# Kernel tuning notes

Hardware: AMD Instinct MI355X
Metric: run time of the kernel (lower is better)

Reference implementation:

```python
import jax, jax.numpy as jnp
import numpy as np
import math

N_CELLS = 8192
IN_DIM = 64
HID = 128
OUT_DIM = 64
MAX_AGE = 50.0
TOP_K = 8


def faction_sync_debate(h, step, n_factions=8, sync_strength=0.15, debate_strength=0.15):
    n, d = h.shape
    n_f = min(n_factions, n // 2)
    if n_f < 2:
        return h
    fs = n // n_f
    used = n_f * fs
    body = h[:used].reshape(n_f, fs, d)
    fmean = body.mean(axis=1, keepdims=True)                 # per-faction mean
    body = (1.0 - sync_strength) * body + sync_strength * fmean
    if step > 5:
        global_op = body.mean(axis=1).mean(axis=0)           # [d]
        dc = max(1, fs // 4)
        body = body.at[:, :dc].set((1.0 - debate_strength) * body[:, :dc] + debate_strength * global_op)
    out = body.reshape(used, d)
    if used < n:
        out = jnp.concatenate([out, h[used:]], axis=0)
    return out


def setup_inputs() -> dict:
    key = jax.random.key(0)
    ks = jax.random.split(key, 10)

    def lin(k, fin, fout):
        kw, kb = jax.random.split(k)
        s = 1.0 / math.sqrt(fin)
        w = jax.random.uniform(kw, (fout, fin), minval=-s, maxval=s, dtype=jnp.float32)
        b = jax.random.uniform(kb, (fout,), minval=-s, maxval=s, dtype=jnp.float32)
        return w, b

    in_w, in_b = lin(ks[0], IN_DIM, HID)
    out_w, out_b = lin(ks[1], HID, IN_DIM)
    ea_w1, ea_b1 = lin(ks[2], HID, 128)
    ea_w2, ea_b2 = lin(ks[3], 128, OUT_DIM)
    eg_w1, eg_b1 = lin(ks[4], HID, 128)
    eg_w2, eg_b2 = lin(ks[5], 128, OUT_DIM)
    prototypes = jax.random.normal(ks[6], (N_CELLS, HID), dtype=jnp.float32) * 0.3
    # sparse random topology state (evolved-state stand-in for the zero-init buffers)
    edges = (jax.random.uniform(ks[7], (N_CELLS, N_CELLS)) < 0.001).astype(jnp.float32)
    edges = jnp.maximum(edges, edges.T)
    edge_ages = jax.random.randint(ks[8], (N_CELLS, N_CELLS), 0, 60).astype(jnp.float32) * edges
    x = jax.random.normal(ks[9], (1, IN_DIM), dtype=jnp.float32)
    return dict(x=x, step=10, prototypes=prototypes, edges=edges, edge_ages=edge_ages,
                in_w=in_w, in_b=in_b, out_w=out_w, out_b=out_b,
                ea_w1=ea_w1, ea_b1=ea_b1, ea_w2=ea_w2, ea_b2=ea_b2,
                eg_w1=eg_w1, eg_b1=eg_b1, eg_w2=eg_w2, eg_b2=eg_b2)


def reference(x, step, prototypes, edges, edge_ages, in_w, in_b, out_w, out_b,
              ea_w1, ea_b1, ea_w2, ea_b2, eg_w1, eg_b1, eg_w2, eg_b2):
    signal = (x @ in_w.T + in_b)[0]                          # [HID]
    # ---- torch.no_grad() region: GNG competitive update ----
    sgp = jax.lax.stop_gradient(prototypes)
    sgs = jax.lax.stop_gradient(signal)
    dists = jnp.sum((sgp - sgs[None, :]) ** 2, axis=-1)      # [N]
    sorted_idx = jnp.argsort(dists)
    bmu1, bmu2 = sorted_idx[0], sorted_idx[1]
    eps_w = max(0.05, 0.3 * math.exp(-step / 200.0))
    eps_n = eps_w * 0.01
    proto = sgp.at[bmu1].add(eps_w * (sgs - sgp[bmu1]))
    proto = proto.at[bmu2].add(eps_n * (sgs - proto[bmu2]))
    e = edges.at[bmu1, bmu2].set(1.0).at[bmu2, bmu1].set(1.0)
    ages = edge_ages.at[bmu1, bmu2].set(0.0).at[bmu2, bmu1].set(0.0)
    ages = ages.at[bmu1, :].add(1.0).at[:, bmu1].add(1.0)
    old = ages > MAX_AGE
    e = jnp.where(old, 0.0, e)
    ages = jnp.where(old, 0.0, ages)
    # vectorized neighbor EMA (replaces per-neighbor python loop; rows independent)
    nmask = (e[bmu1] > 0).astype(proto.dtype)                # [N]
    proto = proto + eps_n * nmask[:, None] * (sgs[None, :] - proto)
    proto = faction_sync_debate(proto, step)
    # value = updated prototypes, grad = identity to the prototypes parameter
    # (torch mutates .data in-place, then reads the Parameter directly)
    proto_used = prototypes + jax.lax.stop_gradient(proto - prototypes)
    # ---- differentiable head ----
    winner_h = proto_used[bmu1][None, :]                     # [1, HID]
    a_out = jax.nn.relu(winner_h @ ea_w1.T + ea_b1) @ ea_w2.T + ea_b2
    g_out = jax.nn.relu(winner_h @ eg_w1.T + eg_b1) @ eg_w2.T + eg_b2
    tension = jnp.mean((a_out - g_out) ** 2)
    top_idx = sorted_idx[:TOP_K]
    weights = jax.nn.softmax(-dists[top_idx])                # [K]
    combined = jnp.sum(weights[:, None] * proto_used[top_idx], axis=0, keepdims=True)
    output = combined @ out_w.T + out_b                      # [1, IN_DIM]
    return output, tension
```

## Files before the change

### kernel.cpp

```cpp
#include <hip/hip_runtime.h>
#include <math.h>

#define N_CELLS 8192
#define HIDDIM 128
#define IN_DIM 64
#define TOPK 8


__global__ void k_init(float* __restrict__ z) {
    int t = blockIdx.x * blockDim.x + threadIdx.x;
    if (t < 2056) z[t] = 0.0f;
}

__global__ __launch_bounds__(128) void k_signal(const float* __restrict__ x,
                                                const float* __restrict__ in_w,
                                                const float* __restrict__ in_b,
                                                float* __restrict__ signal) {
    int j = threadIdx.x;
    float acc = in_b[j];
    const float* w = in_w + j * IN_DIM;
    #pragma unroll
    for (int k = 0; k < IN_DIM; ++k) acc += x[k] * w[k];
    signal[j] = acc;
}

__global__ __launch_bounds__(256) void k_dist(const float* __restrict__ proto,
                                              const float* __restrict__ signal,
                                              float* __restrict__ dists,
                                              float* __restrict__ fsum0) {
    __shared__ float sm[4 * 128];
    int tid = threadIdx.x;
    int wave = tid >> 6, lane = tid & 63;
    float2 s2 = ((const float2*)signal)[lane];
    float fx = 0.0f, fy = 0.0f;
    int base = blockIdx.x * 64;
    for (int c = wave; c < 64; c += 4) {
        int cell = base + c;
        float2 p = ((const float2*)(proto + (size_t)cell * HIDDIM))[lane];
        float dx = p.x - s2.x, dy = p.y - s2.y;
        float d = dx * dx + dy * dy;
        #pragma unroll
        for (int off = 32; off > 0; off >>= 1) d += __shfl_down(d, off, 64);
        if (lane == 0) dists[cell] = d;
        fx += p.x; fy += p.y;
    }
    sm[wave * 128 + 2 * lane]     = fx;
    sm[wave * 128 + 2 * lane + 1] = fy;
    __syncthreads();
    if (tid < 128) {
        float s = sm[tid] + sm[128 + tid] + sm[256 + tid] + sm[384 + tid];
        int f = blockIdx.x >> 4;
        atomicAdd(&fsum0[f * HIDDIM + tid], s);
    }
}

__global__ __launch_bounds__(256) void k_top8(const float* __restrict__ dists,
                                              float* __restrict__ topdist,
                                              int* __restrict__ topidx) {
    __shared__ float sd[N_CELLS];
    __shared__ float sv[256];
    __shared__ int   si[256];
    int tid = threadIdx.x;
    for (int j = 0; j < 32; ++j) sd[j * 256 + tid] = dists[j * 256 + tid];
    __syncthreads();
    for (int k = 0; k < TOPK; ++k) {
        float lv = INFINITY; int li = N_CELLS;
        #pragma unroll
        for (int j = 0; j < 32; ++j) {
            int   ii = j * 256 + tid;
            float vv = sd[ii];
            if (vv < lv || (vv == lv && ii < li)) { lv = vv; li = ii; }
        }
        sv[tid] = lv; si[tid] = li;
        __syncthreads();
        for (int s = 128; s > 0; s >>= 1) {
            if (tid < s) {
                float ov = sv[tid + s]; int oi = si[tid + s];
                if (ov < sv[tid] || (ov == sv[tid] && oi < si[tid])) { sv[tid] = ov; si[tid] = oi; }
            }
            __syncthreads();
        }
        if (tid == 0) {
            topdist[k] = sv[0];
            topidx[k]  = si[0];
            sd[si[0]]  = INFINITY;
        }
        __syncthreads();
    }
}

__global__ __launch_bounds__(256) void k_coef(const float* __restrict__ proto,
                                              const float* __restrict__ edges,
                                              const float* __restrict__ ages,
                                              const int* __restrict__ step_p,
                                              const int* __restrict__ topidx,
                                              float* __restrict__ acoef,
                                              float* __restrict__ csum,
                                              float* __restrict__ Bf) {
    int i = blockIdx.x * blockDim.x + threadIdx.x;
    if (i >= N_CELLS) return;
    int bmu1 = topidx[0], bmu2 = topidx[1];
    float step = (float)step_p[0];
    float eps_w = fmaxf(0.05f, 0.3f * expf(-step / 200.0f));
    float eps_n = eps_w * 0.01f;

    size_t ro = (size_t)bmu1 * N_CELLS + (size_t)i;
    float age, ec;
    if (i == bmu2)      { age = 1.0f;             ec = 1.0f; }
    else if (i == bmu1) { age = ages[ro] + 2.0f;  ec = edges[ro]; }
    else                { age = ages[ro] + 1.0f;  ec = edges[ro]; }
    bool nb = ((age > 50.0f) ? 0.0f : ec) > 0.0f;

    float a = 1.0f;
    if (i == bmu1) a *= (1.0f - eps_w);
    if (i == bmu2) a *= (1.0f - eps_n);
    if (nb)        a *= (1.0f - eps_n);
    acoef[i] = a;

    if (a != 1.0f) {
        int f = i >> 10;
        const float* p = proto + (size_t)i * HIDDIM;
        for (int d = 0; d < HIDDIM; ++d)
            atomicAdd(&csum[f * HIDDIM + d], (a - 1.0f) * p[d]);
        atomicAdd(&Bf[f], 1.0f - a);
    }
}

__global__ __launch_bounds__(128) void k_final(const float* __restrict__ proto,
                                               const float* __restrict__ signal,
                                               const float* __restrict__ acoef,
                                               const float* __restrict__ fsum0,
                                               const float* __restrict__ csum,
                                               const float* __restrict__ Bf,
                                               const float* __restrict__ topdist,
                                               const int* __restrict__ topidx,
                                               const int* __restrict__ step_p,
                                               const float* __restrict__ ea_w1,
                                               const float* __restrict__ ea_b1,
                                               const float* __restrict__ ea_w2,
                                               const float* __restrict__ ea_b2,
                                               const float* __restrict__ eg_w1,
                                               const float* __restrict__ eg_b1,
                                               const float* __restrict__ eg_w2,
                                               const float* __restrict__ eg_b2,
                                               const float* __restrict__ out_w,
                                               const float* __restrict__ out_b,
                                               float* __restrict__ d_out) {
    __shared__ float wh[128], cmb[128], hA[128], hG[128];
    int d = threadIdx.x;
    int step = step_p[0];
    float s = signal[d];

    float fm[8]; float g = 0.0f;
    #pragma unroll
    for (int f = 0; f < 8; ++f) {
        float v = (fsum0[f * 128 + d] + csum[f * 128 + d] + Bf[f] * s) * (1.0f / 1024.0f);
        fm[f] = v; g += v;
    }
    g *= (1.0f / 8.0f);

    float w[TOPK]; float tot = 0.0f; float m = topdist[0];
    #pragma unroll
    for (int k = 0; k < TOPK; ++k) { w[k] = expf(-(topdist[k] - m)); tot += w[k]; }
    float inv = 1.0f / tot;

    float comb = 0.0f, win = 0.0f;
    #pragma unroll
    for (int k = 0; k < TOPK; ++k) {
        int idx = topidx[k];
        float a  = acoef[idx];
        float p1 = a * proto[(size_t)idx * 128 + d] + (1.0f - a) * s;
        float pf = 0.85f * p1 + 0.15f * fm[idx >> 10];
        if (step > 5 && (idx & 1023) < 256) pf = 0.85f * pf + 0.15f * g;
        comb += (w[k] * inv) * pf;
        if (k == 0) win = pf;
    }
    wh[d] = win; cmb[d] = comb;
    __syncthreads();

    float ha = ea_b1[d], hg = eg_b1[d];
    for (int j = 0; j < 128; ++j) {
        ha += wh[j] * ea_w1[d * 128 + j];
        hg += wh[j] * eg_w1[d * 128 + j];
    }
    hA[d] = fmaxf(ha, 0.0f);
    hG[d] = fmaxf(hg, 0.0f);
    __syncthreads();

    if (d < 64) {
        float ao = ea_b2[d], go = eg_b2[d], ov = out_b[d];
        for (int j = 0; j < 128; ++j) {
            ao += hA[j] * ea_w2[d * 128 + j];
            go += hG[j] * eg_w2[d * 128 + j];
            ov += cmb[j] * out_w[d * 128 + j];
        }
        d_out[d] = ov;
        float diff = ao - go;
        float sq = diff * diff;
        #pragma unroll
        for (int off = 32; off > 0; off >>= 1) sq += __shfl_down(sq, off, 64);
        if (d == 0) d_out[64] = sq * (1.0f / 64.0f);
    }
}

extern "C" void kernel_launch(void* const* d_in, const int* in_sizes, int n_in,
                              void* d_out, int out_size, void* d_ws, size_t ws_size,
                              hipStream_t stream) {
    (void)in_sizes; (void)n_in; (void)out_size; (void)ws_size;
    const float* x      = (const float*)d_in[0];
    const int*   step_p = (const int*)  d_in[1];
    const float* proto  = (const float*)d_in[2];
    const float* edges  = (const float*)d_in[3];
    const float* ages   = (const float*)d_in[4];
    const float* in_w   = (const float*)d_in[5];
    const float* in_b   = (const float*)d_in[6];
    const float* out_w  = (const float*)d_in[7];
    const float* out_b  = (const float*)d_in[8];
    const float* ea_w1  = (const float*)d_in[9];
    const float* ea_b1  = (const float*)d_in[10];
    const float* ea_w2  = (const float*)d_in[11];
    const float* ea_b2  = (const float*)d_in[12];
    const float* eg_w1  = (const float*)d_in[13];
    const float* eg_b1  = (const float*)d_in[14];
    const float* eg_w2  = (const float*)d_in[15];
    const float* eg_b2  = (const float*)d_in[16];

    float* ws     = (float*)d_ws;
    float* signal = ws;
    float* dists  = ws + 128;
    float* acoef  = ws + 8320;
    float* fsum0  = ws + 16512;
    float* csum   = ws + 17536;
    float* Bf     = ws + 18560;
    float* topd   = ws + 18568;
    int*   topi   = (int*)(ws + 18576);
    float* out    = (float*)d_out;

    k_init  <<<dim3(9),   dim3(256), 0, stream>>>(fsum0);
    k_signal<<<dim3(1),   dim3(128), 0, stream>>>(x, in_w, in_b, signal);
    k_dist  <<<dim3(128), dim3(256), 0, stream>>>(proto, signal, dists, fsum0);
    k_top8  <<<dim3(1),   dim3(256), 0, stream>>>(dists, topd, topi);
    k_coef  <<<dim3(32),  dim3(256), 0, stream>>>(proto, edges, ages, step_p, topi, acoef, csum, Bf);
    k_final <<<dim3(1),   dim3(128), 0, stream>>>(proto, signal, acoef, fsum0, csum, Bf, topd, topi, step_p,
                                                  ea_w1, ea_b1, ea_w2, ea_b2,
                                                  eg_w1, eg_b1, eg_w2, eg_b2,
                                                  out_w, out_b, out);
}
```

Measured before the change: 488.9 us.

## Fuse top-k with coefficient pass, replace atomics with compacted neighbor list

Drops the zero-init kernel and the global float atomics. k_dist now writes per-block faction partial sums, and k_final reduces them. Top-8 selection and the neighbor-coefficient scan run in one 512-thread block, which compacts the affected cells into a list with a shared-memory counter. The final kernel rebuilds the faction correction from that list and recomputes the top-k coefficients. It also computes the MLP layers with wave-wide coalesced dot products, trading fewer launches and atomics for more serial work in single-block kernels.

```diff
diff --git a/kernel.cpp b/kernel.cpp
--- a/kernel.cpp
+++ b/kernel.cpp
@@ -2,15 +2,8 @@
 #include <math.h>
 
 #define N_CELLS 8192
-#define HIDDIM 128
-#define IN_DIM 64
 #define TOPK 8
 
-
-__global__ void k_init(float* __restrict__ z) {
-    int t = blockIdx.x * blockDim.x + threadIdx.x;
-    if (t < 2056) z[t] = 0.0f;
-}
 
 __global__ __launch_bounds__(128) void k_signal(const float* __restrict__ x,
                                                 const float* __restrict__ in_w,
@@ -18,25 +11,25 @@
                                                 float* __restrict__ signal) {
     int j = threadIdx.x;
     float acc = in_b[j];
-    const float* w = in_w + j * IN_DIM;
+    const float* w = in_w + j * 64;
     #pragma unroll
-    for (int k = 0; k < IN_DIM; ++k) acc += x[k] * w[k];
+    for (int k = 0; k < 64; ++k) acc += x[k] * w[k];
     signal[j] = acc;
 }
 
 __global__ __launch_bounds__(256) void k_dist(const float* __restrict__ proto,
                                               const float* __restrict__ signal,
                                               float* __restrict__ dists,
-                                              float* __restrict__ fsum0) {
-    __shared__ float sm[4 * 128];
+                                              float* __restrict__ partial) {
+    __shared__ float sm[512];
     int tid = threadIdx.x;
     int wave = tid >> 6, lane = tid & 63;
     float2 s2 = ((const float2*)signal)[lane];
     float fx = 0.0f, fy = 0.0f;
-    int base = blockIdx.x * 64;
-    for (int c = wave; c < 64; c += 4) {
+    int base = blockIdx.x * 32;
+    for (int c = wave; c < 32; c += 4) {
         int cell = base + c;
-        float2 p = ((const float2*)(proto + (size_t)cell * HIDDIM))[lane];
+        float2 p = ((const float2*)(proto + (size_t)cell * 128))[lane];
         float dx = p.x - s2.x, dy = p.y - s2.y;
         float d = dx * dx + dy * dy;
         #pragma unroll
@@ -47,93 +40,87 @@
     sm[wave * 128 + 2 * lane]     = fx;
     sm[wave * 128 + 2 * lane + 1] = fy;
     __syncthreads();
-    if (tid < 128) {
-        float s = sm[tid] + sm[128 + tid] + sm[256 + tid] + sm[384 + tid];
-        int f = blockIdx.x >> 4;
-        atomicAdd(&fsum0[f * HIDDIM + tid], s);
-    }
-}
-
-__global__ __launch_bounds__(256) void k_top8(const float* __restrict__ dists,
-                                              float* __restrict__ topdist,
-                                              int* __restrict__ topidx) {
+    if (tid < 128)
+        partial[blockIdx.x * 128 + tid] = sm[tid] + sm[128 + tid] + sm[256 + tid] + sm[384 + tid];
+}
+
+__global__ __launch_bounds__(512) void k_topcoef(const float* __restrict__ dists_g,
+                                                 const float* __restrict__ edges,
+                                                 const float* __restrict__ ages,
+                                                 const int* __restrict__ step_p,
+                                                 float* __restrict__ topd,
+                                                 int* __restrict__ topi,
+                                                 int* __restrict__ nlist,
+                                                 int* __restrict__ listIdx,
+                                                 float* __restrict__ listA) {
     __shared__ float sd[N_CELLS];
-    __shared__ float sv[256];
-    __shared__ int   si[256];
-    int tid = threadIdx.x;
-    for (int j = 0; j < 32; ++j) sd[j * 256 + tid] = dists[j * 256 + tid];
+    __shared__ float sv[512];
+    __shared__ int   si[512];
+    __shared__ int   sbmu[8];
+    __shared__ int   lcnt;
+    int t = threadIdx.x;
+    if (t == 0) lcnt = 0;
+    for (int j = 0; j < 16; ++j) sd[j * 512 + t] = dists_g[j * 512 + t];
     __syncthreads();
     for (int k = 0; k < TOPK; ++k) {
         float lv = INFINITY; int li = N_CELLS;
         #pragma unroll
-        for (int j = 0; j < 32; ++j) {
-            int   ii = j * 256 + tid;
+        for (int j = 0; j < 16; ++j) {
+            int   ii = j * 512 + t;
             float vv = sd[ii];
             if (vv < lv || (vv == lv && ii < li)) { lv = vv; li = ii; }
         }
-        sv[tid] = lv; si[tid] = li;
+        sv[t] = lv; si[t] = li;
         __syncthreads();
-        for (int s = 128; s > 0; s >>= 1) {
-            if (tid < s) {
-                float ov = sv[tid + s]; int oi = si[tid + s];
-                if (ov < sv[tid] || (ov == sv[tid] && oi < si[tid])) { sv[tid] = ov; si[tid] = oi; }
+        for (int s = 256; s > 0; s >>= 1) {
+            if (t < s) {
+                float ov = sv[t + s]; int oi = si[t + s];
+                if (ov < sv[t] || (ov == sv[t] && oi < si[t])) { sv[t] = ov; si[t] = oi; }
             }
             __syncthreads();
         }
-        if (tid == 0) {
-            topdist[k] = sv[0];
-            topidx[k]  = si[0];
-            sd[si[0]]  = INFINITY;
+        if (t == 0) {
+            topd[k] = sv[0]; topi[k] = si[0]; sbmu[k] = si[0];
+            sd[si[0]] = INFINITY;
         }
         __syncthreads();
     }
-}
-
-__global__ __launch_bounds__(256) void k_coef(const float* __restrict__ proto,
-                                              const float* __restrict__ edges,
-                                              const float* __restrict__ ages,
-                                              const int* __restrict__ step_p,
-                                              const int* __restrict__ topidx,
-                                              float* __restrict__ acoef,
-                                              float* __restrict__ csum,
-                                              float* __restrict__ Bf) {
-    int i = blockIdx.x * blockDim.x + threadIdx.x;
-    if (i >= N_CELLS) return;
-    int bmu1 = topidx[0], bmu2 = topidx[1];
+    int bmu1 = sbmu[0], bmu2 = sbmu[1];
     float step = (float)step_p[0];
     float eps_w = fmaxf(0.05f, 0.3f * expf(-step / 200.0f));
     float eps_n = eps_w * 0.01f;
-
-    size_t ro = (size_t)bmu1 * N_CELLS + (size_t)i;
-    float age, ec;
-    if (i == bmu2)      { age = 1.0f;             ec = 1.0f; }
-    else if (i == bmu1) { age = ages[ro] + 2.0f;  ec = edges[ro]; }
-    else                { age = ages[ro] + 1.0f;  ec = edges[ro]; }
-    bool nb = ((age > 50.0f) ? 0.0f : ec) > 0.0f;
-
-    float a = 1.0f;
-    if (i == bmu1) a *= (1.0f - eps_w);
-    if (i == bmu2) a *= (1.0f - eps_n);
-    if (nb)        a *= (1.0f - eps_n);
-    acoef[i] = a;
-
-    if (a != 1.0f) {
-        int f = i >> 10;
-        const float* p = proto + (size_t)i * HIDDIM;
-        for (int d = 0; d < HIDDIM; ++d)
-            atomicAdd(&csum[f * HIDDIM + d], (a - 1.0f) * p[d]);
-        atomicAdd(&Bf[f], 1.0f - a);
-    }
-}
-
-__global__ __launch_bounds__(128) void k_final(const float* __restrict__ proto,
+    const float* erow = edges + (size_t)bmu1 * N_CELLS;
+    const float* arow = ages  + (size_t)bmu1 * N_CELLS;
+    for (int i = t; i < N_CELLS; i += 512) {
+        float age, ec;
+        if (i == bmu2)      { age = 1.0f;          ec = 1.0f; }
+        else if (i == bmu1) { age = arow[i] + 2.0f; ec = erow[i]; }
+        else                { age = arow[i] + 1.0f; ec = erow[i]; }
+        bool nb = ((age > 50.0f) ? 0.0f : ec) > 0.0f;
+        float a = 1.0f;
+        if (i == bmu1) a *= (1.0f - eps_w);
+        if (i == bmu2) a *= (1.0f - eps_n);
+        if (nb)        a *= (1.0f - eps_n);
+        if (a != 1.0f) {
+            int pos = atomicAdd(&lcnt, 1);
+            listIdx[pos] = i;
+            listA[pos]   = a;
+        }
+    }
+    __syncthreads();
+    if (t == 0) *nlist = lcnt;
+}
+
+__global__ __launch_bounds__(256) void k_final(const float* __restrict__ proto,
                                                const float* __restrict__ signal,
-                                               const float* __restrict__ acoef,
-                                               const float* __restrict__ fsum0,
-                                               const float* __restrict__ csum,
-                                               const float* __restrict__ Bf,
-                                               const float* __restrict__ topdist,
-                                               const int* __restrict__ topidx,
+                                               const float* __restrict__ partial,
+                                               const float* __restrict__ topd_g,
+                                               const int* __restrict__ topi_g,
+                                               const int* __restrict__ nlist,
+                                               const int* __restrict__ listIdx,
+                                               const float* __restrict__ listA,
+                                               const float* __restrict__ edges,
+                                               const float* __restrict__ ages,
                                                const int* __restrict__ step_p,
                                                const float* __restrict__ ea_w1,
                                                const float* __restrict__ ea_b1,
@@ -146,60 +133,122 @@
                                                const float* __restrict__ out_w,
                                                const float* __restrict__ out_b,
                                                float* __restrict__ d_out) {
-    __shared__ float wh[128], cmb[128], hA[128], hG[128];
-    int d = threadIdx.x;
+    __shared__ __align__(16) float csumS[1024];
+    __shared__ __align__(16) float fmS[1024];
+    __shared__ float BfS[8];
+    __shared__ __align__(16) float wh[128];
+    __shared__ __align__(16) float cmb[128];
+    __shared__ __align__(16) float hA[128];
+    __shared__ __align__(16) float hG[128];
+    __shared__ float aout[64], gout[64];
+    __shared__ float tda[8];
+    __shared__ int   tia[8];
+    int t = threadIdx.x;
+    int n = *nlist;
     int step = step_p[0];
-    float s = signal[d];
-
-    float fm[8]; float g = 0.0f;
-    #pragma unroll
-    for (int f = 0; f < 8; ++f) {
-        float v = (fsum0[f * 128 + d] + csum[f * 128 + d] + Bf[f] * s) * (1.0f / 1024.0f);
-        fm[f] = v; g += v;
-    }
-    g *= (1.0f / 8.0f);
-
-    float w[TOPK]; float tot = 0.0f; float m = topdist[0];
-    #pragma unroll
-    for (int k = 0; k < TOPK; ++k) { w[k] = expf(-(topdist[k] - m)); tot += w[k]; }
-    float inv = 1.0f / tot;
-
-    float comb = 0.0f, win = 0.0f;
-    #pragma unroll
-    for (int k = 0; k < TOPK; ++k) {
-        int idx = topidx[k];
-        float a  = acoef[idx];
-        float p1 = a * proto[(size_t)idx * 128 + d] + (1.0f - a) * s;
-        float pf = 0.85f * p1 + 0.15f * fm[idx >> 10];
-        if (step > 5 && (idx & 1023) < 256) pf = 0.85f * pf + 0.15f * g;
-        comb += (w[k] * inv) * pf;
-        if (k == 0) win = pf;
-    }
-    wh[d] = win; cmb[d] = comb;
-    __syncthreads();
-
-    float ha = ea_b1[d], hg = eg_b1[d];
-    for (int j = 0; j < 128; ++j) {
-        ha += wh[j] * ea_w1[d * 128 + j];
-        hg += wh[j] * eg_w1[d * 128 + j];
-    }
-    hA[d] = fmaxf(ha, 0.0f);
-    hG[d] = fmaxf(hg, 0.0f);
-    __syncthreads();
-
-    if (d < 64) {
-        float ao = ea_b2[d], go = eg_b2[d], ov = out_b[d];
-        for (int j = 0; j < 128; ++j) {
-            ao += hA[j] * ea_w2[d * 128 + j];
-            go += hG[j] * eg_w2[d * 128 + j];
-            ov += cmb[j] * out_w[d * 128 + j];
-        }
-        d_out[d] = ov;
-        float diff = ao - go;
+    if (t < 8) { tda[t] = topd_g[t]; tia[t] = topi_g[t]; }
+    if (t < 128) {
+        #pragma unroll
+        for (int f = 0; f < 8; ++f) csumS[f * 128 + t] = 0.0f;
+    }
+    __syncthreads();
+    if (t < 128) {
+        int d = t;
+        for (int e = 0; e < n; ++e) {
+            int idx = listIdx[e]; float a = listA[e];
+            csumS[(idx >> 10) * 128 + d] += (a - 1.0f) * proto[(size_t)idx * 128 + d];
+        }
+    } else if (t < 136) {
+        int f = t - 128; float acc = 0.0f;
+        for (int e = 0; e < n; ++e)
+            if ((listIdx[e] >> 10) == f) acc += 1.0f - listA[e];
+        BfS[f] = acc;
+    }
+    __syncthreads();
+    if (t < 128) {
+        int d = t;
+        float s = signal[d];
+        float g = 0.0f;
+        #pragma unroll
+        for (int f = 0; f < 8; ++f) {
+            float acc = 0.0f;
+            for (int b = 0; b < 32; ++b) acc += partial[(f * 32 + b) * 128 + d];
+            float v = (acc + csumS[f * 128 + d] + BfS[f] * s) * (1.0f / 1024.0f);
+            fmS[f * 128 + d] = v; g += v;
+        }
+        g *= 0.125f;
+        float wk[TOPK]; float tot = 0.0f; float m = tda[0];
+        #pragma unroll
+        for (int k = 0; k < TOPK; ++k) { wk[k] = expf(-(tda[k] - m)); tot += wk[k]; }
+        float inv = 1.0f / tot;
+        int bmu1 = tia[0], bmu2 = tia[1];
+        float stf = (float)step;
+        float eps_w = fmaxf(0.05f, 0.3f * expf(-stf / 200.0f));
+        float eps_n = eps_w * 0.01f;
+        float comb = 0.0f, win = 0.0f;
+        #pragma unroll
+        for (int k = 0; k < TOPK; ++k) {
+            int idx = tia[k];
+            size_t ro = (size_t)bmu1 * N_CELLS + (size_t)idx;
+            float age, ec;
+            if (idx == bmu2)      { age = 1.0f;            ec = 1.0f; }
+            else if (idx == bmu1) { age = ages[ro] + 2.0f;  ec = edges[ro]; }
+            else                  { age = ages[ro] + 1.0f;  ec = edges[ro]; }
+            bool nb = ((age > 50.0f) ? 0.0f : ec) > 0.0f;
+            float a = 1.0f;
+            if (idx == bmu1) a *= (1.0f - eps_w);
+            if (idx == bmu2) a *= (1.0f - eps_n);
+            if (nb)          a *= (1.0f - eps_n);
+            float p1 = a * proto[(size_t)idx * 128 + d] + (1.0f - a) * s;
+            float pf = 0.85f * p1 + 0.15f * fmS[(idx >> 10) * 128 + d];
+            if (step > 5 && (idx & 1023) < 256) pf = 0.85f * pf + 0.15f * g;
+            comb += wk[k] * inv * pf;
+            if (k == 0) win = pf;
+        }
+        wh[d] = win; cmb[d] = comb;
+    }
+    __syncthreads();
+    int wave = t >> 6, lane = t & 63;
+    for (int q = 0; q < 64; ++q) {
+        int task = wave * 64 + q;
+        int row = task & 127;
+        const float* W = (task < 128) ? ea_w1 : eg_w1;
+        float2 wv = ((const float2*)(W + row * 128))[lane];
+        float2 hv = ((const float2*)wh)[lane];
+        float acc = wv.x * hv.x + wv.y * hv.y;
+        #pragma unroll
+        for (int off = 32; off > 0; off >>= 1) acc += __shfl_down(acc, off, 64);
+        if (lane == 0) {
+            float b = (task < 128) ? ea_b1[row] : eg_b1[row];
+            float h = fmaxf(acc + b, 0.0f);
+            if (task < 128) hA[row] = h; else hG[row] = h;
+        }
+    }
+    __syncthreads();
+    for (int q = 0; q < 48; ++q) {
+        int task = wave + 4 * q;
+        int row; const float* W; const float* hsrc;
+        if (task < 64)       { row = task;       W = ea_w2; hsrc = hA;  }
+        else if (task < 128) { row = task - 64;  W = eg_w2; hsrc = hG;  }
+        else                 { row = task - 128; W = out_w; hsrc = cmb; }
+        float2 wv = ((const float2*)(W + row * 128))[lane];
+        float2 hv = ((const float2*)hsrc)[lane];
+        float acc = wv.x * hv.x + wv.y * hv.y;
+        #pragma unroll
+        for (int off = 32; off > 0; off >>= 1) acc += __shfl_down(acc, off, 64);
+        if (lane == 0) {
+            if (task < 64)       aout[row] = acc + ea_b2[row];
+            else if (task < 128) gout[row] = acc + eg_b2[row];
+            else                 d_out[row] = acc + out_b[row];
+        }
+    }
+    __syncthreads();
+    if (t < 64) {
+        float diff = aout[t] - gout[t];
         float sq = diff * diff;
         #pragma unroll
         for (int off = 32; off > 0; off >>= 1) sq += __shfl_down(sq, off, 64);
-        if (d == 0) d_out[64] = sq * (1.0f / 64.0f);
+        if (t == 0) d_out[64] = sq * (1.0f / 64.0f);
     }
 }
 
@@ -225,24 +274,24 @@
     const float* eg_w2  = (const float*)d_in[15];
     const float* eg_b2  = (const float*)d_in[16];
 
-    float* ws     = (float*)d_ws;
-    float* signal = ws;
-    float* dists  = ws + 128;
-    float* acoef  = ws + 8320;
-    float* fsum0  = ws + 16512;
-    float* csum   = ws + 17536;
-    float* Bf     = ws + 18560;
-    float* topd   = ws + 18568;
-    int*   topi   = (int*)(ws + 18576);
-    float* out    = (float*)d_out;
-
-    k_init  <<<dim3(9),   dim3(256), 0, stream>>>(fsum0);
-    k_signal<<<dim3(1),   dim3(128), 0, stream>>>(x, in_w, in_b, signal);
-    k_dist  <<<dim3(128), dim3(256), 0, stream>>>(proto, signal, dists, fsum0);
-    k_top8  <<<dim3(1),   dim3(256), 0, stream>>>(dists, topd, topi);
-    k_coef  <<<dim3(32),  dim3(256), 0, stream>>>(proto, edges, ages, step_p, topi, acoef, csum, Bf);
-    k_final <<<dim3(1),   dim3(128), 0, stream>>>(proto, signal, acoef, fsum0, csum, Bf, topd, topi, step_p,
-                                                  ea_w1, ea_b1, ea_w2, ea_b2,
-                                                  eg_w1, eg_b1, eg_w2, eg_b2,
-                                                  out_w, out_b, out);
-}
+    float* ws      = (float*)d_ws;
+    float* signal  = ws;
+    float* dists   = ws + 128;
+    float* partial = ws + 8320;
+    float* topd    = ws + 41088;
+    int*   topi    = (int*)(ws + 41096);
+    int*   nlist   = (int*)(ws + 41104);
+    int*   listIdx = (int*)(ws + 41112);
+    float* listA   = ws + 49304;
+    float* out     = (float*)d_out;
+
+    k_signal <<<dim3(1),   dim3(128), 0, stream>>>(x, in_w, in_b, signal);
+    k_dist   <<<dim3(256), dim3(256), 0, stream>>>(proto, signal, dists, partial);
+    k_topcoef<<<dim3(1),   dim3(512), 0, stream>>>(dists, edges, ages, step_p,
+                                                   topd, topi, nlist, listIdx, listA);
+    k_final  <<<dim3(1),   dim3(256), 0, stream>>>(proto, signal, partial, topd, topi,
+                                                   nlist, listIdx, listA, edges, ages, step_p,
+                                                   ea_w1, ea_b1, ea_w2, ea_b2,
+                                                   eg_w1, eg_b1, eg_w2, eg_b2,
+                                                   out_w, out_b, out);
+}
```

Result: slower. 570.5 us (+16.7%).
